# Performance work log

Measured on AMD Instinct MI355X. Metric: run time of the kernel, lower is better.

Reference implementation:

```python
import jax, jax.numpy as jnp
import numpy as np

L, B, E, H = 1024, 8, 1024, 16
HD = E // H
SCALE = HD ** -0.5
EPS = 1e-5


def setup_inputs() -> dict:
    key = jax.random.key(0)
    ks = jax.random.split(key, 6)
    s = E ** -0.5
    return {
        "x": jax.random.normal(ks[0], (L, B, E), dtype=jnp.float32),
        "attn_mask": jnp.zeros((L, L), dtype=jnp.float32),
        "Wq": jax.random.normal(ks[1], (E, E), dtype=jnp.float32) * s,
        "bq": jnp.zeros((E,), dtype=jnp.float32),
        "Wk": jax.random.normal(ks[2], (E, E), dtype=jnp.float32) * s,
        "bk": jnp.zeros((E,), dtype=jnp.float32),
        "Wv": jax.random.normal(ks[3], (E, E), dtype=jnp.float32) * s,
        "bv": jnp.zeros((E,), dtype=jnp.float32),
        "Wo": jax.random.normal(ks[4], (E, E), dtype=jnp.float32) * s,
        "bo": jnp.zeros((E,), dtype=jnp.float32),
        "gamma": jnp.ones((E,), dtype=jnp.float32),
        "beta": jnp.zeros((E,), dtype=jnp.float32),
    }


def _layernorm(x, gamma, beta):
    mu = jnp.mean(x, axis=-1, keepdims=True)
    var = jnp.mean(jnp.square(x - mu), axis=-1, keepdims=True)
    return (x - mu) * jax.lax.rsqrt(var + EPS) * gamma + beta


def reference(x, attn_mask, Wq, bq, Wk, bk, Wv, bv, Wo, bo, gamma, beta):
    # x: (L, B, E); pre-LN residual attention block (dropout=0, eval)
    ln_x = _layernorm(x, gamma, beta)
    # torch Linear: y = x @ W.T + b
    q = (ln_x @ Wq.T + bq) * SCALE
    k = ln_x @ Wk.T + bk
    v = ln_x @ Wv.T + bv
    # (L, B, E) -> (B, H, L, hd)
    def split_heads(t):
        return t.reshape(L, B, H, HD).transpose(1, 2, 0, 3)
    q, k, v = split_heads(q), split_heads(k), split_heads(v)
    # full attention matrix, as in the original non-fused bmm path
    attn = jnp.einsum('bhqd,bhkd->bhqk', q, k) + attn_mask[None, None]
    attn = jax.nn.softmax(attn, axis=-1)
    out = jnp.einsum('bhqk,bhkd->bhqd', attn, v)  # (B, H, L, hd)
    out = out.transpose(2, 0, 1, 3).reshape(L, B, E)
    out = out @ Wo.T + bo
    return x + out
```

## Files before the change

kernel.cpp:

```cpp
#include <hip/hip_runtime.h>

#define LL 1024
#define BB 8
#define EE 1024
#define HH 16
#define HD 64
#define MROWS (LL*BB)

typedef __attribute__((ext_vector_type(8))) short short8v;
typedef __attribute__((ext_vector_type(4))) float f32x4;
typedef __attribute__((ext_vector_type(16))) float f32x16;

#define LOG2E 1.44269504088896f

__device__ __forceinline__ unsigned short tobf(float f) {
    union { float f; unsigned u; } un; un.f = f;
    unsigned u = un.u;
    u += 0x7fffu + ((u >> 16) & 1u);
    return (unsigned short)(u >> 16);
}

__device__ __forceinline__ float max3f(float a, float b, float c) {
    return fmaxf(fmaxf(a, b), c);
}

__device__ __forceinline__ void load_lds16(const unsigned short* g, unsigned short* l) {
    __builtin_amdgcn_global_load_lds((const __attribute__((address_space(1))) unsigned int*)g,
                                     (__attribute__((address_space(3))) unsigned int*)l,
                                     16, 0, 0);
}

__global__ __launch_bounds__(256) void convw4_kernel(const float* __restrict__ w0,
                                                     const float* __restrict__ w1,
                                                     const float* __restrict__ w2,
                                                     const float* __restrict__ w3,
                                                     unsigned short* __restrict__ o0,
                                                     unsigned short* __restrict__ o1,
                                                     unsigned short* __restrict__ o2,
                                                     unsigned short* __restrict__ o3) {
    const float* w; unsigned short* o;
    switch (blockIdx.y) {
        case 0:  w = w0; o = o0; break;
        case 1:  w = w1; o = o1; break;
        case 2:  w = w2; o = o2; break;
        default: w = w3; o = o3; break;
    }
    int i = (blockIdx.x * 256 + threadIdx.x) * 4;
    float4 v = *(const float4*)&w[i];
    ushort4 r;
    r.x = tobf(v.x); r.y = tobf(v.y); r.z = tobf(v.z); r.w = tobf(v.w);
    *(ushort4*)&o[i] = r;
}

__global__ __launch_bounds__(256) void maskprep_kernel(const float* __restrict__ m,
                                                       unsigned* __restrict__ o) {
    __shared__ float t_sh[64][65];
    const int q0 = blockIdx.x * 64, k0 = blockIdx.y * 64;
    const int tid = threadIdx.x;
    {
        const int r = tid >> 2, c0 = (tid & 3) * 16;
        #pragma unroll
        for (int i = 0; i < 4; ++i) {
            float4 v = *(const float4*)&m[(size_t)(q0 + r) * LL + k0 + c0 + i*4];
            t_sh[r][c0+i*4+0] = v.x; t_sh[r][c0+i*4+1] = v.y;
            t_sh[r][c0+i*4+2] = v.z; t_sh[r][c0+i*4+3] = v.w;
        }
    }
    __syncthreads();
    const int k2l = tid >> 3, qi = (tid & 7) * 8;
    unsigned pk[8];
    #pragma unroll
    for (int j = 0; j < 8; ++j) {
        const unsigned lo = tobf(t_sh[qi+j][2*k2l]   * LOG2E);
        const unsigned hb = tobf(t_sh[qi+j][2*k2l+1] * LOG2E);
        pk[j] = lo | (hb << 16);
    }
    unsigned* orow = &o[(size_t)(k0/2 + k2l) * LL + q0 + qi];
    *(uint4*)&orow[0] = make_uint4(pk[0], pk[1], pk[2], pk[3]);
    *(uint4*)&orow[4] = make_uint4(pk[4], pk[5], pk[6], pk[7]);
}

__global__ __launch_bounds__(256) void ln_kernel(const float* __restrict__ x,
                                                 const float* __restrict__ gamma,
                                                 const float* __restrict__ beta,
                                                 unsigned short* __restrict__ out) {
    const int row = blockIdx.x;
    const int tid = threadIdx.x;
    const float4 v = *(const float4*)&x[(size_t)row * EE + tid * 4];
    float s = v.x + v.y + v.z + v.w;
    float q = v.x*v.x + v.y*v.y + v.z*v.z + v.w*v.w;
    #pragma unroll
    for (int off = 1; off < 64; off <<= 1) {
        s += __shfl_xor(s, off);
        q += __shfl_xor(q, off);
    }
    __shared__ float ss[4], sq[4];
    const int wv = tid >> 6;
    if ((tid & 63) == 0) { ss[wv] = s; sq[wv] = q; }
    __syncthreads();
    s = ss[0] + ss[1] + ss[2] + ss[3];
    q = sq[0] + sq[1] + sq[2] + sq[3];
    const float mu = s * (1.0f / EE);
    const float var = q * (1.0f / EE) - mu * mu;
    const float rs = rsqrtf(var + 1e-5f);
    ushort4 o;
    o.x = tobf((v.x - mu) * rs * gamma[tid*4+0] + beta[tid*4+0]);
    o.y = tobf((v.y - mu) * rs * gamma[tid*4+1] + beta[tid*4+1]);
    o.z = tobf((v.z - mu) * rs * gamma[tid*4+2] + beta[tid*4+2]);
    o.w = tobf((v.w - mu) * rs * gamma[tid*4+3] + beta[tid*4+3]);
    *(ushort4*)&out[(size_t)row * EE + tid * 4] = o;
}

#define GEMM128_BODY(A_, W_)                                                              \
    __shared__ unsigned short a_sh[3][128*32];                                            \
    __shared__ unsigned short b_sh[3][128*32];                                            \
    const int tid = threadIdx.x, lane = tid & 63, wave = tid >> 6;                        \
    const int bm = blockIdx.y * 128, bn = blockIdx.x * 128;                               \
    const int wr = (wave >> 1) * 64, wc = (wave & 1) * 64;                                \
    const int l16 = lane & 15, q4 = lane >> 4;                                            \
    const int grow = lane >> 2;                                                           \
    const int gswz = (((lane & 3) ^ (grow & 3)) * 8);                                     \
    const int rslot = (q4 ^ (l16 & 3)) * 16;                       \
    f32x4 acc[4][4] = {};                                                                 \
                                                           \
    _Pragma("unroll")                                                                     \
    for (int i = 0; i < 2; ++i) {                                                         \
        const int ch = wave * 2 + i;                                                      \
        load_lds16(&A_[(size_t)(bm + ch*16 + grow)*EE + gswz], &a_sh[0][ch*512]);         \
        load_lds16(&W_[(size_t)(bn + ch*16 + grow)*EE + gswz], &b_sh[0][ch*512]);         \
    }                                                                                     \
    _Pragma("unroll")                                                                     \
    for (int i = 0; i < 2; ++i) {                                                         \
        const int ch = wave * 2 + i;                                                      \
        load_lds16(&A_[(size_t)(bm + ch*16 + grow)*EE + 32 + gswz], &a_sh[1][ch*512]);    \
        load_lds16(&W_[(size_t)(bn + ch*16 + grow)*EE + 32 + gswz], &b_sh[1][ch*512]);    \
    }                                                                                     \
    int buf = 0, sb = 2;                                                                  \
    for (int it = 0; it < 32; ++it) {                                                     \
        if (it < 31) asm volatile("s_waitcnt vmcnt(4)" ::: "memory");                     \
        else         asm volatile("s_waitcnt vmcnt(0)" ::: "memory");                     \
        __builtin_amdgcn_s_barrier();                                                     \
        if (it < 30) {                                                                    \
            const int kn = (it + 2) * 32;                                                 \
            _Pragma("unroll")                                                             \
            for (int i = 0; i < 2; ++i) {                                                 \
                const int ch = wave * 2 + i;                                              \
                load_lds16(&A_[(size_t)(bm + ch*16 + grow)*EE + kn + gswz], &a_sh[sb][ch*512]); \
                load_lds16(&W_[(size_t)(bn + ch*16 + grow)*EE + kn + gswz], &b_sh[sb][ch*512]); \
            }                                                                             \
        }                                                                                 \
        short8v af[4], bf[4];                                                             \
        _Pragma("unroll")                                                                 \
        for (int mi = 0; mi < 4; ++mi)                                                    \
            af[mi] = *(const short8v*)((const char*)&a_sh[buf][0] + (size_t)(wr + mi*16 + l16)*64 + rslot); \
        _Pragma("unroll")                                                                 \
        for (int ni = 0; ni < 4; ++ni)                                                    \
            bf[ni] = *(const short8v*)((const char*)&b_sh[buf][0] + (size_t)(wc + ni*16 + l16)*64 + rslot); \
        __builtin_amdgcn_s_setprio(1);                                                    \
        _Pragma("unroll")                                                                 \
        for (int mi = 0; mi < 4; ++mi)                                                    \
            _Pragma("unroll")                                                             \
            for (int ni = 0; ni < 4; ++ni)                                                \
                acc[mi][ni] = __builtin_amdgcn_mfma_f32_16x16x32_bf16(af[mi], bf[ni], acc[mi][ni], 0, 0, 0); \
        __builtin_amdgcn_s_setprio(0);                                                    \
        buf = (buf == 2) ? 0 : buf + 1;                                                   \
        sb  = (sb  == 2) ? 0 : sb  + 1;                                                   \
    }

__global__ __launch_bounds__(256) void gemm_qkv(const unsigned short* __restrict__ A,
                                                const unsigned short* __restrict__ W,
                                                const float* __restrict__ bq,
                                                const float* __restrict__ bk,
                                                const float* __restrict__ bv,
                                                unsigned short* __restrict__ qo,
                                                unsigned short* __restrict__ ko,
                                                unsigned short* __restrict__ vo) {
    GEMM128_BODY(A, W)
    const int seg = blockIdx.x >> 3;
    const float* bias = seg == 0 ? bq : (seg == 1 ? bk : bv);
    #pragma unroll
    for (int mi = 0; mi < 4; ++mi) {
        #pragma unroll
        for (int ni = 0; ni < 4; ++ni) {
            #pragma unroll
            for (int r = 0; r < 4; ++r) {
                const int m  = bm + wr + mi*16 + (lane >> 4)*4 + r;
                const int nn = (bn & 1023) + wc + ni*16 + l16;
                const float v = acc[mi][ni][r] + bias[nn];
                const int l = m >> 3, b = m & 7, h = nn >> 6, d = nn & 63;
                if (seg == 0)      qo[((size_t)(b*HH + h) * LL + l) * HD + d] = tobf(v * (0.125f * LOG2E));
                else if (seg == 1) ko[((size_t)(b*HH + h) * LL + l) * HD + d] = tobf(v);
                else               vo[((size_t)(b*HH + h) * HD + d) * LL + l] = tobf(v);
            }
        }
    }
}

__global__ __launch_bounds__(256) void gemm_o(const unsigned short* __restrict__ A,
                                              const unsigned short* __restrict__ W,
                                              const float* __restrict__ bias,
                                              const float* __restrict__ xres,
                                              float* __restrict__ outf) {
    GEMM128_BODY(A, W)
    #pragma unroll
    for (int mi = 0; mi < 4; ++mi) {
        #pragma unroll
        for (int ni = 0; ni < 4; ++ni) {
            #pragma unroll
            for (int r = 0; r < 4; ++r) {
                const int m = bm + wr + mi*16 + (lane >> 4)*4 + r;
                const int n = bn + wc + ni*16 + l16;
                outf[(size_t)m * EE + n] = acc[mi][ni][r] + bias[n] + xres[(size_t)m * EE + n];
            }
        }
    }
}

__global__ __launch_bounds__(256) void attn_kernel(const unsigned short* __restrict__ qarr,
                                                   const unsigned short* __restrict__ karr,
                                                   const unsigned short* __restrict__ vtarr,
                                                   const unsigned* __restrict__ maskT2,
                                                   unsigned short* __restrict__ attn_out) {
    __shared__ __attribute__((aligned(16))) unsigned short k_sh[3][64*64];
    __shared__ __attribute__((aligned(16))) unsigned short v_sh[3][64*64];
    const int tid = threadIdx.x, lane = tid & 63, wave = tid >> 6;
    const int l32 = lane & 31, hi = lane >> 5;
    const int bh = blockIdx.y;
    const int qtok = blockIdx.x * 128 + wave * 32 + l32;
    const unsigned short* qb = qarr  + (size_t)bh * LL * HD;
    const unsigned short* kb = karr  + (size_t)bh * LL * HD;
    const unsigned short* vb = vtarr + (size_t)bh * HD * LL;

    short8v qf[4];
    #pragma unroll
    for (int dc = 0; dc < 4; ++dc)
        qf[dc] = *(const short8v*)&qb[(size_t)qtok * HD + dc*16 + hi*8];

    f32x16 acc[2] = {};
    float mrun = -1e30f, srun = 0.f;

    auto stage = [&](int bufi, int kv) {
        #pragma unroll
        for (int i = 0; i < 2; ++i) {
            const int r = wave*16 + i*8 + (lane >> 3);
            const int c = ((lane & 7) ^ (r & 7)) * 8;
            load_lds16(&kb[(size_t)(kv + r) * HD + c], &k_sh[bufi][(wave*16 + i*8) * 64]);
            load_lds16(&vb[(size_t)r * LL + kv + c],   &v_sh[bufi][(wave*16 + i*8) * 64]);
        }
    };

    auto finish = [&](f32x16& s, const unsigned* mu, int sub, int bufi) {
        #pragma unroll
        for (int j = 0; j < 8; ++j) {
            s[2*j]   += __uint_as_float(mu[j] << 16);
            s[2*j+1] += __uint_as_float(mu[j] & 0xffff0000u);
        }
        const float a0 = max3f(s[0],  s[1],  s[2]);
        const float a1 = max3f(s[3],  s[4],  s[5]);
        const float a2 = max3f(s[6],  s[7],  s[8]);
        const float a3 = max3f(s[9],  s[10], s[11]);
        const float a4 = max3f(s[12], s[13], s[14]);
        float pm = fmaxf(max3f(a0, a1, a2), max3f(a3, a4, s[15]));
        pm = fmaxf(pm, __shfl_xor(pm, 32));
        if (__any(pm - mrun > 8.0f)) {
            const float mn = fmaxf(mrun, pm);
            const float al = exp2f(mrun - mn);
            #pragma unroll
            for (int i = 0; i < 16; ++i) { acc[0][i] *= al; acc[1][i] *= al; }
            srun *= al;
            mrun = mn;
        }
        float p[16];
        #pragma unroll
        for (int i = 0; i < 16; ++i) p[i] = exp2f(s[i] - mrun);
        const float t0 = p[0]+p[1],   t1 = p[2]+p[3],   t2 = p[4]+p[5],   t3 = p[6]+p[7];
        const float t4 = p[8]+p[9],   t5 = p[10]+p[11], t6 = p[12]+p[13], t7 = p[14]+p[15];
        const float u0 = t0+t1, u1 = t2+t3, u2 = t4+t5, u3 = t6+t7;
        float rs = (u0+u1) + (u2+u3);
        rs += __shfl_xor(rs, 32);
        srun += rs;
        unsigned w[8];
        #pragma unroll
        for (int j = 0; j < 8; ++j)
            asm("v_cvt_pk_bf16_f32 %0, %1, %2" : "=v"(w[j]) : "v"(p[2*j]), "v"(p[2*j+1]));
        asm volatile("v_permlane32_swap_b32 %0, %1" : "+v"(w[0]), "+v"(w[2]));
        asm volatile("v_permlane32_swap_b32 %0, %1" : "+v"(w[1]), "+v"(w[3]));
        asm volatile("v_permlane32_swap_b32 %0, %1" : "+v"(w[4]), "+v"(w[6]));
        asm volatile("v_permlane32_swap_b32 %0, %1" : "+v"(w[5]), "+v"(w[7]));
        union { uint4 u; short8v s8; } pb0, pb1;
        pb0.u = make_uint4(w[0], w[1], w[2], w[3]);
        pb1.u = make_uint4(w[4], w[5], w[6], w[7]);
        __builtin_amdgcn_s_setprio(1);
        #pragma unroll
        for (int dt = 0; dt < 2; ++dt) {
            const int row = dt*32 + l32;
            const short8v vf0 = *(const short8v*)((const char*)&v_sh[bufi][0]
                                  + (size_t)row*128 + ((((sub*2+0)*2 + hi) ^ (l32 & 7)) * 16));
            const short8v vf1 = *(const short8v*)((const char*)&v_sh[bufi][0]
                                  + (size_t)row*128 + ((((sub*2+1)*2 + hi) ^ (l32 & 7)) * 16));
            acc[dt] = __builtin_amdgcn_mfma_f32_32x32x16_bf16(vf0, pb0.s8, acc[dt], 0, 0, 0);
            acc[dt] = __builtin_amdgcn_mfma_f32_32x32x16_bf16(vf1, pb1.s8, acc[dt], 0, 0, 0);
        }
        __builtin_amdgcn_s_setprio(0);
    };

    const unsigned* mt2base = maskT2 + qtok;
    stage(0, 0);
    unsigned mcur[16], mnxt[16];
    #pragma unroll
    for (int j = 0; j < 8; ++j) {
        mcur[j]     = mt2base[(size_t)((j & 1) + 4*(j >> 1) + 2*hi) * LL];
        mcur[8 + j] = mt2base[(size_t)(16 + (j & 1) + 4*(j >> 1) + 2*hi) * LL];
    }
    stage(1, 64);

    const int NT = LL / 64;
    int buf = 0, sb = 2;
    for (int t = 0; t < NT; ++t) {
        if (t < NT - 1) asm volatile("s_waitcnt vmcnt(4)" ::: "memory");
        else            asm volatile("s_waitcnt vmcnt(0)" ::: "memory");
        __builtin_amdgcn_s_barrier();
        if (t < NT - 1) {
            const unsigned* mt2n = mt2base + (size_t)(t + 1) * 32 * LL;
            #pragma unroll
            for (int j = 0; j < 8; ++j) {
                mnxt[j]     = mt2n[(size_t)((j & 1) + 4*(j >> 1) + 2*hi) * LL];
                mnxt[8 + j] = mt2n[(size_t)(16 + (j & 1) + 4*(j >> 1) + 2*hi) * LL];
            }
        }
        if (t + 2 < NT) stage(sb, (t + 2) * 64);

        f32x16 s0 = {}, s1 = {};
        __builtin_amdgcn_s_setprio(1);
        #pragma unroll
        for (int dc = 0; dc < 4; ++dc) {
            const short8v kf = *(const short8v*)((const char*)&k_sh[buf][0]
                                 + (size_t)(l32)*128 + (((dc*2 + hi) ^ (l32 & 7)) * 16));
            s0 = __builtin_amdgcn_mfma_f32_32x32x16_bf16(kf, qf[dc], s0, 0, 0, 0);
        }
        #pragma unroll
        for (int dc = 0; dc < 4; ++dc) {
            const short8v kf = *(const short8v*)((const char*)&k_sh[buf][0]
                                 + (size_t)(32 + l32)*128 + (((dc*2 + hi) ^ (l32 & 7)) * 16));
            s1 = __builtin_amdgcn_mfma_f32_32x32x16_bf16(kf, qf[dc], s1, 0, 0, 0);
        }
        __builtin_amdgcn_s_setprio(0);
        finish(s0, &mcur[0], 0, buf);
        finish(s1, &mcur[8], 1, buf);
        #pragma unroll
        for (int j = 0; j < 16; ++j) mcur[j] = mnxt[j];
        buf = (buf == 2) ? 0 : buf + 1;
        sb  = (sb  == 2) ? 0 : sb  + 1;
    }
    const float inv = 1.0f / srun;
    const int b = bh >> 4, h = bh & 15;
    unsigned short* orow = attn_out + ((size_t)qtok * BB + b) * EE + h * HD;
    #pragma unroll
    for (int dt = 0; dt < 2; ++dt) {
        #pragma unroll
        for (int g = 0; g < 4; ++g) {
            const float a0 = acc[dt][4*g+0]*inv, a1 = acc[dt][4*g+1]*inv;
            const float a2 = acc[dt][4*g+2]*inv, a3 = acc[dt][4*g+3]*inv;
            unsigned lo, hw;
            asm("v_cvt_pk_bf16_f32 %0, %1, %2" : "=v"(lo) : "v"(a0), "v"(a1));
            asm("v_cvt_pk_bf16_f32 %0, %1, %2" : "=v"(hw) : "v"(a2), "v"(a3));
            *(uint2*)&orow[dt*32 + g*8 + hi*4] = make_uint2(lo, hw);
        }
    }
}

extern "C" void kernel_launch(void* const* d_in, const int* in_sizes, int n_in,
                              void* d_out, int out_size, void* d_ws, size_t ws_size,
                              hipStream_t stream) {
    (void)in_sizes; (void)n_in; (void)out_size; (void)ws_size;
    const float* x     = (const float*)d_in[0];
    const float* mask  = (const float*)d_in[1];
    const float* Wq    = (const float*)d_in[2];
    const float* bq    = (const float*)d_in[3];
    const float* Wk    = (const float*)d_in[4];
    const float* bk    = (const float*)d_in[5];
    const float* Wv    = (const float*)d_in[6];
    const float* bv    = (const float*)d_in[7];
    const float* Wo    = (const float*)d_in[8];
    const float* bo    = (const float*)d_in[9];
    const float* gamma = (const float*)d_in[10];
    const float* beta  = (const float*)d_in[11];
    float* out = (float*)d_out;

    unsigned short* ws   = (unsigned short*)d_ws;
    unsigned short* ln   = ws;
    unsigned short* wqkv = ln   + (size_t)MROWS * EE;
    unsigned short* wob  = wqkv + (size_t)3 * EE * EE;
    unsigned short* qb   = wob  + (size_t)EE * EE;
    unsigned short* kbp  = qb   + (size_t)BB * HH * LL * HD;
    unsigned short* vtb  = kbp  + (size_t)BB * HH * LL * HD;
    unsigned short* attnb = ln;
    unsigned* maskT2 = (unsigned*)wqkv;

    convw4_kernel<<<dim3(1024, 4), 256, 0, stream>>>(
        Wq, Wk, Wv, Wo,
        wqkv, wqkv + (size_t)EE * EE, wqkv + (size_t)2 * EE * EE, wob);
    ln_kernel<<<MROWS, 256, 0, stream>>>(x, gamma, beta, ln);

    gemm_qkv<<<dim3(24, 64), 256, 0, stream>>>(ln, wqkv, bq, bk, bv, qb, kbp, vtb);

    maskprep_kernel<<<dim3(16, 16), 256, 0, stream>>>(mask, maskT2);

    attn_kernel<<<dim3(LL / 128, BB * HH), 256, 0, stream>>>(qb, kbp, vtb, maskT2, attnb);

    gemm_o<<<dim3(8, 64), 256, 0, stream>>>(attnb, wob, bo, x, out);
}
```

Measured before the change: 239.8 us.

## Replace QKV GEMM with 256x256-tile, 8-wave kernel and swizzled block mapping

The QKV projection GEMM now uses 256x256 output tiles with 512 threads (8 waves, each computing 128x64), in place of 128x128 tiles with 4 waves. That raises arithmetic intensity per LDS byte and reduces global reloads of A and W. It adds a split-phase schedule where A and B stage loads interleave with two MFMA half-batches, plus a remapped block index to improve L2 locality. In exchange it uses more registers and LDS per block and launches only 384 blocks, which may limit occupancy or leave compute units underused.

```diff
diff --git a/kernel.cpp b/kernel.cpp
--- a/kernel.cpp
+++ b/kernel.cpp
@@ -111,6 +111,119 @@
     *(ushort4*)&out[(size_t)row * EE + tid * 4] = o;
 }
 
+__global__ __launch_bounds__(512, 2) void gemm_qkv256(const unsigned short* __restrict__ A,
+                                                      const unsigned short* __restrict__ W,
+                                                      const float* __restrict__ bq,
+                                                      const float* __restrict__ bkb,
+                                                      const float* __restrict__ bvb,
+                                                      unsigned short* __restrict__ qo,
+                                                      unsigned short* __restrict__ ko,
+                                                      unsigned short* __restrict__ vo) {
+    __shared__ __attribute__((aligned(16))) unsigned short a_sh[3][256*32];
+    __shared__ __attribute__((aligned(16))) unsigned short b_sh[3][256*32];
+    const int tid = threadIdx.x, lane = tid & 63, wave = tid >> 6;
+    const int wm = wave >> 2, wn = wave & 3;
+    const int l16 = lane & 15, q4 = lane >> 4;
+    const int v   = (blockIdx.x & 7) * 48 + (blockIdx.x >> 3);
+    const int by  = (v / 48) * 4 + (v & 3);
+    const int bx  = (v % 48) >> 2;
+    const int bm  = by * 256, bn = bx * 256;
+    const int srow  = lane >> 2;
+    const int sslot = ((lane & 3) ^ (srow & 3)) * 8;
+    const int rdsl  = (l16 & 3);
+
+    auto stageA = [&](int d, int t) {
+        #pragma unroll
+        for (int i = 0; i < 2; ++i) {
+            const int win = wave * 2 + i;
+            load_lds16(&A[(size_t)(bm + win*16 + srow) * EE + t*32 + sslot],
+                       &a_sh[d][win * 512]);
+        }
+    };
+    auto stageB = [&](int d, int t) {
+        #pragma unroll
+        for (int i = 0; i < 2; ++i) {
+            const int win = wave * 2 + i;
+            load_lds16(&W[(size_t)(bn + win*16 + srow) * EE + t*32 + sslot],
+                       &b_sh[d][win * 512]);
+        }
+    };
+
+    f32x4 acc[8][4] = {};
+    stageA(0, 0); stageB(0, 0);
+    stageA(1, 1); stageB(1, 1);
+
+    int bufc = 0;
+    for (int t = 0; t < 32; ++t) {
+        if (t < 31) asm volatile("s_waitcnt vmcnt(4)" ::: "memory");
+        else        asm volatile("s_waitcnt vmcnt(0)" ::: "memory");
+        __builtin_amdgcn_s_barrier();
+        const int sbuf = (bufc + 2 >= 3) ? bufc - 1 : bufc + 2;
+        if (t + 2 < 32) stageA(sbuf, t + 2);
+        short8v bf[4], af[4];
+        #pragma unroll
+        for (int ni = 0; ni < 4; ++ni) {
+            const int rB = wn*64 + ni*16 + l16;
+            bf[ni] = *(const short8v*)((const char*)&b_sh[bufc][0]
+                        + (size_t)rB*64 + ((q4 ^ rdsl) * 16));
+        }
+        #pragma unroll
+        for (int mi = 0; mi < 4; ++mi) {
+            const int rA = wm*128 + mi*16 + l16;
+            af[mi] = *(const short8v*)((const char*)&a_sh[bufc][0]
+                        + (size_t)rA*64 + ((q4 ^ rdsl) * 16));
+        }
+        __builtin_amdgcn_s_barrier();
+        asm volatile("s_waitcnt lgkmcnt(0)" ::: "memory");
+        __builtin_amdgcn_sched_barrier(0);
+        __builtin_amdgcn_s_setprio(1);
+        #pragma unroll
+        for (int mi = 0; mi < 4; ++mi)
+            #pragma unroll
+            for (int ni = 0; ni < 4; ++ni)
+                acc[mi][ni] = __builtin_amdgcn_mfma_f32_16x16x32_bf16(af[mi], bf[ni], acc[mi][ni], 0, 0, 0);
+        __builtin_amdgcn_s_setprio(0);
+        __builtin_amdgcn_s_barrier();
+        if (t + 2 < 32) stageB(sbuf, t + 2);
+        #pragma unroll
+        for (int mi = 0; mi < 4; ++mi) {
+            const int rA = wm*128 + (mi + 4)*16 + l16;
+            af[mi] = *(const short8v*)((const char*)&a_sh[bufc][0]
+                        + (size_t)rA*64 + ((q4 ^ rdsl) * 16));
+        }
+        __builtin_amdgcn_s_barrier();
+        asm volatile("s_waitcnt lgkmcnt(0)" ::: "memory");
+        __builtin_amdgcn_sched_barrier(0);
+        __builtin_amdgcn_s_setprio(1);
+        #pragma unroll
+        for (int mi = 0; mi < 4; ++mi)
+            #pragma unroll
+            for (int ni = 0; ni < 4; ++ni)
+                acc[mi + 4][ni] = __builtin_amdgcn_mfma_f32_16x16x32_bf16(af[mi], bf[ni], acc[mi + 4][ni], 0, 0, 0);
+        __builtin_amdgcn_s_setprio(0);
+        __builtin_amdgcn_s_barrier();
+        bufc = (bufc + 1 == 3) ? 0 : bufc + 1;
+    }
+    const int seg = bn >> 10;
+    const float* bias = seg == 0 ? bq : (seg == 1 ? bkb : bvb);
+    #pragma unroll
+    for (int mi = 0; mi < 8; ++mi) {
+        #pragma unroll
+        for (int ni = 0; ni < 4; ++ni) {
+            #pragma unroll
+            for (int r = 0; r < 4; ++r) {
+                const int m  = bm + wm*128 + mi*16 + q4*4 + r;
+                const int nn = (bn & 1023) + wn*64 + ni*16 + l16;
+                const float vv = acc[mi][ni][r] + bias[nn];
+                const int l = m >> 3, b = m & 7, h = nn >> 6, d = nn & 63;
+                if (seg == 0)      qo[((size_t)(b*HH + h) * LL + l) * HD + d] = tobf(vv * (0.125f * LOG2E));
+                else if (seg == 1) ko[((size_t)(b*HH + h) * LL + l) * HD + d] = tobf(vv);
+                else               vo[((size_t)(b*HH + h) * HD + d) * LL + l] = tobf(vv);
+            }
+        }
+    }
+}
+
 #define GEMM128_BODY(A_, W_)                                                              \
     __shared__ unsigned short a_sh[3][128*32];                                            \
     __shared__ unsigned short b_sh[3][128*32];                                            \
@@ -122,7 +235,6 @@
     const int gswz = (((lane & 3) ^ (grow & 3)) * 8);                                     \
     const int rslot = (q4 ^ (l16 & 3)) * 16;                       \
     f32x4 acc[4][4] = {};                                                                 \
-                                                           \
     _Pragma("unroll")                                                                     \
     for (int i = 0; i < 2; ++i) {                                                         \
         const int ch = wave * 2 + i;                                                      \
@@ -167,35 +279,6 @@
         sb  = (sb  == 2) ? 0 : sb  + 1;                                                   \
     }
 
-__global__ __launch_bounds__(256) void gemm_qkv(const unsigned short* __restrict__ A,
-                                                const unsigned short* __restrict__ W,
-                                                const float* __restrict__ bq,
-                                                const float* __restrict__ bk,
-                                                const float* __restrict__ bv,
-                                                unsigned short* __restrict__ qo,
-                                                unsigned short* __restrict__ ko,
-                                                unsigned short* __restrict__ vo) {
-    GEMM128_BODY(A, W)
-    const int seg = blockIdx.x >> 3;
-    const float* bias = seg == 0 ? bq : (seg == 1 ? bk : bv);
-    #pragma unroll
-    for (int mi = 0; mi < 4; ++mi) {
-        #pragma unroll
-        for (int ni = 0; ni < 4; ++ni) {
-            #pragma unroll
-            for (int r = 0; r < 4; ++r) {
-                const int m  = bm + wr + mi*16 + (lane >> 4)*4 + r;
-                const int nn = (bn & 1023) + wc + ni*16 + l16;
-                const float v = acc[mi][ni][r] + bias[nn];
-                const int l = m >> 3, b = m & 7, h = nn >> 6, d = nn & 63;
-                if (seg == 0)      qo[((size_t)(b*HH + h) * LL + l) * HD + d] = tobf(v * (0.125f * LOG2E));
-                else if (seg == 1) ko[((size_t)(b*HH + h) * LL + l) * HD + d] = tobf(v);
-                else               vo[((size_t)(b*HH + h) * HD + d) * LL + l] = tobf(v);
-            }
-        }
-    }
-}
-
 __global__ __launch_bounds__(256) void gemm_o(const unsigned short* __restrict__ A,
                                               const unsigned short* __restrict__ W,
                                               const float* __restrict__ bias,
@@ -402,7 +485,7 @@
         wqkv, wqkv + (size_t)EE * EE, wqkv + (size_t)2 * EE * EE, wob);
     ln_kernel<<<MROWS, 256, 0, stream>>>(x, gamma, beta, ln);
 
-    gemm_qkv<<<dim3(24, 64), 256, 0, stream>>>(ln, wqkv, bq, bk, bv, qb, kbp, vtb);
+    gemm_qkv256<<<384, 512, 0, stream>>>(ln, wqkv, bq, bk, bv, qb, kbp, vtb);
 
     maskprep_kernel<<<dim3(16, 16), 256, 0, stream>>>(mask, maskT2);
 
```

New measurement: 278.4 us. +16.1%, slower.

## Store Q/K/V in MFMA fragment layout and load attention operands directly without LDS

Applied to the files above, without the earlier changes.

The QKV GEMM epilogue now writes Q, K and V in a pre-swizzled fragment-major layout, so each lane can load its MFMA operand as one contiguous 16-byte vector. The attention kernel drops LDS staging, barriers and the triple buffer. It reads K/V fragments straight from global memory (relying on L2 reuse across the four waves), processes 32 keys per step, and remaps the grid to a 1D launch that places the 8 batches' blocks for one head next to each other. This removes LDS traffic and synchronisation, at the cost of redundant global/L2 loads per wave and a shorter prefetch distance that may expose memory latency.

```diff
diff --git a/kernel.cpp b/kernel.cpp
--- a/kernel.cpp
+++ b/kernel.cpp
@@ -122,7 +122,6 @@
     const int gswz = (((lane & 3) ^ (grow & 3)) * 8);                                     \
     const int rslot = (q4 ^ (l16 & 3)) * 16;                       \
     f32x4 acc[4][4] = {};                                                                 \
-                                                           \
     _Pragma("unroll")                                                                     \
     for (int i = 0; i < 2; ++i) {                                                         \
         const int ch = wave * 2 + i;                                                      \
@@ -188,9 +187,18 @@
                 const int nn = (bn & 1023) + wc + ni*16 + l16;
                 const float v = acc[mi][ni][r] + bias[nn];
                 const int l = m >> 3, b = m & 7, h = nn >> 6, d = nn & 63;
-                if (seg == 0)      qo[((size_t)(b*HH + h) * LL + l) * HD + d] = tobf(v * (0.125f * LOG2E));
-                else if (seg == 1) ko[((size_t)(b*HH + h) * LL + l) * HD + d] = tobf(v);
-                else               vo[((size_t)(b*HH + h) * HD + d) * LL + l] = tobf(v);
+                const int bh = b*HH + h;
+                if (seg == 2) {
+                    const int k16 = l >> 4, khi = (l >> 3) & 1, ke = l & 7;
+                    const int dt = d >> 5, dl = d & 31;
+                    vo[((((size_t)bh*64 + k16)*2 + dt)*64 + khi*32 + dl)*8 + ke] = tobf(v);
+                } else {
+                    const int t32 = l >> 5, l32 = l & 31;
+                    const int dc = d >> 4, hi2 = (d >> 3) & 1, e = d & 7;
+                    const size_t idx = ((((size_t)bh*32 + t32)*4 + dc)*64 + hi2*32 + l32)*8 + e;
+                    if (seg == 0) qo[idx] = tobf(v * (0.125f * LOG2E));
+                    else          ko[idx] = tobf(v);
+                }
             }
         }
     }
@@ -216,44 +224,63 @@
     }
 }
 
-__global__ __launch_bounds__(256) void attn_kernel(const unsigned short* __restrict__ qarr,
-                                                   const unsigned short* __restrict__ karr,
-                                                   const unsigned short* __restrict__ vtarr,
+__global__ __launch_bounds__(256) void attn_kernel(const unsigned short* __restrict__ Qf,
+                                                   const unsigned short* __restrict__ Kf,
+                                                   const unsigned short* __restrict__ Vf,
                                                    const unsigned* __restrict__ maskT2,
                                                    unsigned short* __restrict__ attn_out) {
-    __shared__ __attribute__((aligned(16))) unsigned short k_sh[3][64*64];
-    __shared__ __attribute__((aligned(16))) unsigned short v_sh[3][64*64];
     const int tid = threadIdx.x, lane = tid & 63, wave = tid >> 6;
     const int l32 = lane & 31, hi = lane >> 5;
-    const int bh = blockIdx.y;
-    const int qtok = blockIdx.x * 128 + wave * 32 + l32;
-    const unsigned short* qb = qarr  + (size_t)bh * LL * HD;
-    const unsigned short* kb = karr  + (size_t)bh * LL * HD;
-    const unsigned short* vb = vtarr + (size_t)bh * HD * LL;
+    const int b1 = blockIdx.x;
+    const int bh = (b1 & 7) * 16 + ((b1 >> 3) & 15);
+    const int qt = ((b1 >> 7) & 7) * 4 + wave;
+    const int qtok = qt * 32 + l32;
+    const unsigned short* qfp = Qf + ((size_t)(bh * 32 + qt) * 4) * 512;
+    const unsigned short* kfb = Kf + (size_t)bh * 32 * 4 * 512;
+    const unsigned short* vfb = Vf + (size_t)bh * 64 * 2 * 512;
 
     short8v qf[4];
     #pragma unroll
     for (int dc = 0; dc < 4; ++dc)
-        qf[dc] = *(const short8v*)&qb[(size_t)qtok * HD + dc*16 + hi*8];
+        qf[dc] = *(const short8v*)&qfp[dc * 512 + lane * 8];
 
     f32x16 acc[2] = {};
     float mrun = -1e30f, srun = 0.f;
 
-    auto stage = [&](int bufi, int kv) {
-        #pragma unroll
-        for (int i = 0; i < 2; ++i) {
-            const int r = wave*16 + i*8 + (lane >> 3);
-            const int c = ((lane & 7) ^ (r & 7)) * 8;
-            load_lds16(&kb[(size_t)(kv + r) * HD + c], &k_sh[bufi][(wave*16 + i*8) * 64]);
-            load_lds16(&vb[(size_t)r * LL + kv + c],   &v_sh[bufi][(wave*16 + i*8) * 64]);
-        }
-    };
-
-    auto finish = [&](f32x16& s, const unsigned* mu, int sub, int bufi) {
+    const unsigned* mt2base = maskT2 + qtok;
+    short8v kf[4];
+    #pragma unroll
+    for (int dc = 0; dc < 4; ++dc)
+        kf[dc] = *(const short8v*)&kfb[dc * 512 + lane * 8];
+    unsigned mcur[8], mnxt[8];
+    #pragma unroll
+    for (int j = 0; j < 8; ++j)
+        mcur[j] = mt2base[(size_t)((j & 1) + 4*(j >> 1) + 2*hi) * LL];
+
+    for (int t = 0; t < 32; ++t) {
+        f32x16 s = {};
+        __builtin_amdgcn_s_setprio(1);
+        #pragma unroll
+        for (int dc = 0; dc < 4; ++dc)
+            s = __builtin_amdgcn_mfma_f32_32x32x16_bf16(kf[dc], qf[dc], s, 0, 0, 0);
+        __builtin_amdgcn_s_setprio(0);
+        short8v vf00, vf01, vf10, vf11;
+        vf00 = *(const short8v*)&vfb[((size_t)(t*2 + 0)*2 + 0)*512 + lane*8];
+        vf01 = *(const short8v*)&vfb[((size_t)(t*2 + 0)*2 + 1)*512 + lane*8];
+        vf10 = *(const short8v*)&vfb[((size_t)(t*2 + 1)*2 + 0)*512 + lane*8];
+        vf11 = *(const short8v*)&vfb[((size_t)(t*2 + 1)*2 + 1)*512 + lane*8];
+        if (t < 31) {
+            #pragma unroll
+            for (int dc = 0; dc < 4; ++dc)
+                kf[dc] = *(const short8v*)&kfb[((size_t)(t + 1)*4 + dc)*512 + lane*8];
+            #pragma unroll
+            for (int j = 0; j < 8; ++j)
+                mnxt[j] = mt2base[(size_t)((t + 1)*16 + (j & 1) + 4*(j >> 1) + 2*hi) * LL];
+        }
         #pragma unroll
         for (int j = 0; j < 8; ++j) {
-            s[2*j]   += __uint_as_float(mu[j] << 16);
-            s[2*j+1] += __uint_as_float(mu[j] & 0xffff0000u);
+            s[2*j]   += __uint_as_float(mcur[j] << 16);
+            s[2*j+1] += __uint_as_float(mcur[j] & 0xffff0000u);
         }
         const float a0 = max3f(s[0],  s[1],  s[2]);
         const float a1 = max3f(s[3],  s[4],  s[5]);
@@ -291,66 +318,13 @@
         pb0.u = make_uint4(w[0], w[1], w[2], w[3]);
         pb1.u = make_uint4(w[4], w[5], w[6], w[7]);
         __builtin_amdgcn_s_setprio(1);
-        #pragma unroll
-        for (int dt = 0; dt < 2; ++dt) {
-            const int row = dt*32 + l32;
-            const short8v vf0 = *(const short8v*)((const char*)&v_sh[bufi][0]
-                                  + (size_t)row*128 + ((((sub*2+0)*2 + hi) ^ (l32 & 7)) * 16));
-            const short8v vf1 = *(const short8v*)((const char*)&v_sh[bufi][0]
-                                  + (size_t)row*128 + ((((sub*2+1)*2 + hi) ^ (l32 & 7)) * 16));
-            acc[dt] = __builtin_amdgcn_mfma_f32_32x32x16_bf16(vf0, pb0.s8, acc[dt], 0, 0, 0);
-            acc[dt] = __builtin_amdgcn_mfma_f32_32x32x16_bf16(vf1, pb1.s8, acc[dt], 0, 0, 0);
-        }
+        acc[0] = __builtin_amdgcn_mfma_f32_32x32x16_bf16(vf00, pb0.s8, acc[0], 0, 0, 0);
+        acc[1] = __builtin_amdgcn_mfma_f32_32x32x16_bf16(vf01, pb0.s8, acc[1], 0, 0, 0);
+        acc[0] = __builtin_amdgcn_mfma_f32_32x32x16_bf16(vf10, pb1.s8, acc[0], 0, 0, 0);
+        acc[1] = __builtin_amdgcn_mfma_f32_32x32x16_bf16(vf11, pb1.s8, acc[1], 0, 0, 0);
         __builtin_amdgcn_s_setprio(0);
-    };
-
-    const unsigned* mt2base = maskT2 + qtok;
-    stage(0, 0);
-    unsigned mcur[16], mnxt[16];
-    #pragma unroll
-    for (int j = 0; j < 8; ++j) {
-        mcur[j]     = mt2base[(size_t)((j & 1) + 4*(j >> 1) + 2*hi) * LL];
-        mcur[8 + j] = mt2base[(size_t)(16 + (j & 1) + 4*(j >> 1) + 2*hi) * LL];
-    }
-    stage(1, 64);
-
-    const int NT = LL / 64;
-    int buf = 0, sb = 2;
-    for (int t = 0; t < NT; ++t) {
-        if (t < NT - 1) asm volatile("s_waitcnt vmcnt(4)" ::: "memory");
-        else            asm volatile("s_waitcnt vmcnt(0)" ::: "memory");
-        __builtin_amdgcn_s_barrier();
-        if (t < NT - 1) {
-            const unsigned* mt2n = mt2base + (size_t)(t + 1) * 32 * LL;
-            #pragma unroll
-            for (int j = 0; j < 8; ++j) {
-                mnxt[j]     = mt2n[(size_t)((j & 1) + 4*(j >> 1) + 2*hi) * LL];
-                mnxt[8 + j] = mt2n[(size_t)(16 + (j & 1) + 4*(j >> 1) + 2*hi) * LL];
-            }
-        }
-        if (t + 2 < NT) stage(sb, (t + 2) * 64);
-
-        f32x16 s0 = {}, s1 = {};
-        __builtin_amdgcn_s_setprio(1);
-        #pragma unroll
-        for (int dc = 0; dc < 4; ++dc) {
-            const short8v kf = *(const short8v*)((const char*)&k_sh[buf][0]
-                                 + (size_t)(l32)*128 + (((dc*2 + hi) ^ (l32 & 7)) * 16));
-            s0 = __builtin_amdgcn_mfma_f32_32x32x16_bf16(kf, qf[dc], s0, 0, 0, 0);
-        }
-        #pragma unroll
-        for (int dc = 0; dc < 4; ++dc) {
-            const short8v kf = *(const short8v*)((const char*)&k_sh[buf][0]
-                                 + (size_t)(32 + l32)*128 + (((dc*2 + hi) ^ (l32 & 7)) * 16));
-            s1 = __builtin_amdgcn_mfma_f32_32x32x16_bf16(kf, qf[dc], s1, 0, 0, 0);
-        }
-        __builtin_amdgcn_s_setprio(0);
-        finish(s0, &mcur[0], 0, buf);
-        finish(s1, &mcur[8], 1, buf);
-        #pragma unroll
-        for (int j = 0; j < 16; ++j) mcur[j] = mnxt[j];
-        buf = (buf == 2) ? 0 : buf + 1;
-        sb  = (sb  == 2) ? 0 : sb  + 1;
+        #pragma unroll
+        for (int j = 0; j < 8; ++j) mcur[j] = mnxt[j];
     }
     const float inv = 1.0f / srun;
     const int b = bh >> 4, h = bh & 15;
@@ -406,7 +380,7 @@
 
     maskprep_kernel<<<dim3(16, 16), 256, 0, stream>>>(mask, maskT2);
 
-    attn_kernel<<<dim3(LL / 128, BB * HH), 256, 0, stream>>>(qb, kbp, vtb, maskT2, attnb);
+    attn_kernel<<<1024, 256, 0, stream>>>(qb, kbp, vtb, maskT2, attnb);
 
     gemm_o<<<dim3(8, 64), 256, 0, stream>>>(attnb, wob, bo, x, out);
 }
```

New measurement: 223.3 us. 1.07x faster.
